# Kernel tuning notes

Hardware: AMD Instinct MI355X
Metric: run time of the kernel (lower is better)

The kernel has to match this reference:

```python
import jax, jax.numpy as jnp
import numpy as np

B, S, D_IN = 4, 2048, 1024
D_OUT, H = 1024, 16
HD = D_OUT // H  # head_dim = 64

def setup_inputs() -> dict:
    key = jax.random.key(0)
    ks = jax.random.split(key, 6)
    scale_in = 1.0 / np.sqrt(D_IN)
    scale_out = 1.0 / np.sqrt(D_OUT)
    return {
        "x": jax.random.normal(ks[0], (B, S, D_IN), dtype=jnp.float32),
        "Wq": jax.random.uniform(ks[1], (D_OUT, D_IN), jnp.float32, -scale_in, scale_in),
        "Wk": jax.random.uniform(ks[2], (D_OUT, D_IN), jnp.float32, -scale_in, scale_in),
        "Wv": jax.random.uniform(ks[3], (D_OUT, D_IN), jnp.float32, -scale_in, scale_in),
        "Wo": jax.random.uniform(ks[4], (D_OUT, D_OUT), jnp.float32, -scale_out, scale_out),
        "bo": jax.random.uniform(ks[5], (D_OUT,), jnp.float32, -scale_out, scale_out),
    }

def reference(x, Wq, Wk, Wv, Wo, bo):
    b, s, _ = x.shape
    # projections (nn.Linear: x @ W.T), split into heads -> [b, h, s, hd]
    def proj(W):
        return jnp.einsum('bsd,ed->bse', x, W).reshape(b, s, H, HD).transpose(0, 2, 1, 3)
    q, k, v = proj(Wq), proj(Wk), proj(Wv)
    # full score matrix [b, h, s, s] with causal mask, scaled softmax
    scores = jnp.einsum('bhqd,bhkd->bhqk', q, k)
    causal = jnp.tril(jnp.ones((s, s), dtype=bool))
    scores = jnp.where(causal, scores, -jnp.inf)
    attn = jax.nn.softmax(scores / np.sqrt(HD), axis=-1)
    # dropout p=0.0 -> identity
    ctx = jnp.einsum('bhqk,bhkd->bqhd', attn, v).reshape(b, s, D_OUT)
    return jnp.einsum('bsd,ed->bse', ctx, Wo) + bo
```

## Files before the change

kernel.cpp:

```cpp
#include <hip/hip_runtime.h>
#include <cstdint>
#include <cstddef>

#define S_LEN   2048
#define D_MODEL 1024
#define N_HEADS 16
#define HEAD_DIM 64
#define BATCH   4
#define M_ROWS  (BATCH * S_LEN)

typedef _Float16 half8  __attribute__((ext_vector_type(8)));
typedef _Float16 half4v __attribute__((ext_vector_type(4)));
typedef float    float4v __attribute__((ext_vector_type(4)));

#define AS1 __attribute__((address_space(1)))
#define AS3 __attribute__((address_space(3)))

#define QSCL 0.1803368801111832f

__device__ __forceinline__ int swz(int row, int byteInRow) {
    return row * 128 + ((((byteInRow >> 4) ^ (row & 7)) << 4)) + (byteInRow & 15);
}

__device__ __forceinline__ int vperm(int a) {
    return (a & 0x20) | ((a & 0x0C) << 1) | ((a & 0x10) >> 2) | (a & 3);
}

__global__ __launch_bounds__(256) void cvt_all(const float* __restrict__ x,
                                               const float* __restrict__ wq,
                                               const float* __restrict__ wk,
                                               const float* __restrict__ wv,
                                               const float* __restrict__ wo,
                                               _Float16* __restrict__ dst) {
    const int NX = M_ROWS * D_MODEL / 4;
    const int NW = D_MODEL * D_MODEL / 4;
    int i = blockIdx.x * 256 + threadIdx.x;
    int j = i;
    const float4v* src;
    if (j < NX) src = (const float4v*)x;
    else {
        j -= NX;
        if (j < NW) src = (const float4v*)wq;
        else { j -= NW;
            if (j < NW) src = (const float4v*)wk;
            else { j -= NW;
                if (j < NW) src = (const float4v*)wv;
                else { j -= NW; src = (const float4v*)wo; }
            }
        }
    }
    float4v v = src[j];
    half4v h;
    h[0] = (_Float16)v[0]; h[1] = (_Float16)v[1];
    h[2] = (_Float16)v[2]; h[3] = (_Float16)v[3];
    ((half4v*)dst)[i] = h;
}

#define GK   1024
#define GNT  16
#define BUFB 49152
#define GEMM_LDS (3 * BUFB)

template <int MODE>
__global__ __launch_bounds__(512, 2) void gemm8p(const _Float16* __restrict__ A,
                                                 const _Float16* __restrict__ Bw,
                                                 _Float16* __restrict__ O1,
                                                 _Float16* __restrict__ O2,
                                                 float* __restrict__ Of,
                                                 const float* __restrict__ bias,
                                                 int N) {
    extern __shared__ char smem[];

    const int tid  = threadIdx.x;
    const int wave = tid >> 6;
    const int lane = tid & 63;
    const int quad = lane >> 4;
    const int l16  = lane & 15;
    const int wm   = wave >> 1;
    const int wn   = wave & 1;

    const int rowBase = blockIdx.x * 256;
    const int colBase = blockIdx.y * 128;

    const int srow = tid >> 3;
    const int csw  = ((tid & 7) ^ (srow & 7)) * 8;
    const _Float16* aS[4];
    const _Float16* bS[2];
#pragma unroll
    for (int i = 0; i < 4; ++i)
        aS[i] = A + (size_t)(rowBase + i * 64 + srow) * GK + csw;
#pragma unroll
    for (int j = 0; j < 2; ++j)
        bS[j] = Bw + (size_t)(colBase + j * 64 + srow) * GK + csw;
    const int dstOff = tid * 16;

    auto stage = [&](int kt, int part) {
        char* base = smem + (kt % 3) * BUFB;
        const size_t ko = (size_t)kt * 64;
        if (part == 0) {
            __builtin_amdgcn_global_load_lds((const AS1 void*)(aS[0] + ko),
                (AS3 void*)(base + 0 * 8192 + dstOff), 16, 0, 0);
            __builtin_amdgcn_global_load_lds((const AS1 void*)(aS[1] + ko),
                (AS3 void*)(base + 1 * 8192 + dstOff), 16, 0, 0);
            __builtin_amdgcn_global_load_lds((const AS1 void*)(bS[0] + ko),
                (AS3 void*)(base + 32768 + dstOff), 16, 0, 0);
        } else {
            __builtin_amdgcn_global_load_lds((const AS1 void*)(aS[2] + ko),
                (AS3 void*)(base + 2 * 8192 + dstOff), 16, 0, 0);
            __builtin_amdgcn_global_load_lds((const AS1 void*)(aS[3] + ko),
                (AS3 void*)(base + 3 * 8192 + dstOff), 16, 0, 0);
            __builtin_amdgcn_global_load_lds((const AS1 void*)(bS[1] + ko),
                (AS3 void*)(base + 32768 + 8192 + dstOff), 16, 0, 0);
        }
    };

    const int aRow = (wm * 64 + l16) * 128;
    const int bRow = (wn * 64 + l16) * 128;
    int swzk[2];
    swzk[0] = ((quad)     ^ (l16 & 7)) << 4;
    swzk[1] = ((quad + 4) ^ (l16 & 7)) << 4;

    float4v acc[4][4] = {};

    stage(0, 0); stage(0, 1); stage(1, 0); stage(1, 1);
    asm volatile("s_waitcnt vmcnt(6)" ::: "memory");
    __builtin_amdgcn_s_barrier();

#pragma unroll
    for (int kt = 0; kt < GNT; ++kt) {
        const char* Ab = smem + (kt % 3) * BUFB;
        const char* Bb = Ab + 32768;
#pragma unroll
        for (int ks = 0; ks < 2; ++ks) {
            half8 af[4], bf[4];
#pragma unroll
            for (int mi = 0; mi < 4; ++mi)
                af[mi] = *(const half8*)(Ab + aRow + mi * 2048 + swzk[ks]);
#pragma unroll
            for (int ni = 0; ni < 4; ++ni)
                bf[ni] = *(const half8*)(Bb + bRow + ni * 2048 + swzk[ks]);
            if (kt + 2 < GNT) stage(kt + 2, ks);
            __builtin_amdgcn_s_barrier();
            asm volatile("s_waitcnt lgkmcnt(0)" ::: "memory");
            __builtin_amdgcn_sched_barrier(0);
            __builtin_amdgcn_s_setprio(1);
#pragma unroll
            for (int mi = 0; mi < 4; ++mi)
#pragma unroll
                for (int ni = 0; ni < 4; ++ni)
                    acc[mi][ni] = __builtin_amdgcn_mfma_f32_16x16x32_f16(
                        af[mi], bf[ni], acc[mi][ni], 0, 0, 0);
            __builtin_amdgcn_s_setprio(0);
            if (ks == 1) {
                if (kt + 2 < GNT) {
                    asm volatile("s_waitcnt vmcnt(6)" ::: "memory");
                } else if (kt + 1 < GNT) {
                    asm volatile("s_waitcnt vmcnt(0)" ::: "memory");
                }
            }
            __builtin_amdgcn_s_barrier();
        }
    }

    const int rowOff = wm * 64;
    const int colOff = wn * 64;
#pragma unroll
    for (int mi = 0; mi < 4; ++mi)
#pragma unroll
        for (int ni = 0; ni < 4; ++ni) {
            const int col = colBase + colOff + ni * 16 + l16;
#pragma unroll
            for (int i = 0; i < 4; ++i) {
                const int row = rowBase + rowOff + mi * 16 + quad * 4 + i;
                float v = acc[mi][ni][i];
                if (MODE == 0) {
                    int b_ = row >> 11, s_ = row & 2047;
                    int proj = col >> 10, d = col & 1023;
                    int h_ = d >> 6, hd = d & 63;
                    _Float16* dst = proj ? O2 : O1;
                    if (proj == 0) v *= QSCL;
                    dst[(((size_t)(b_ * 16 + h_) * 2048 + s_) << 6) + hd] = (_Float16)v;
                } else if (MODE == 1) {
                    int h_ = row >> 6, hd = row & 63;
                    int b_ = col >> 11, s_ = col & 2047;
                    int sp = (s_ & ~63) | vperm(s_ & 63);
                    O1[(((size_t)(b_ * 16 + h_) * 64 + hd) << 11) + sp] = (_Float16)v;
                } else {
                    Of[(size_t)row * N + col] = v + bias[col];
                }
            }
        }
}

template <bool MASKED>
__device__ __forceinline__ void softmax_side(const float4v (&sT)[2][4], int krow0,
                                             int qt, int quad, int c,
                                             half8 (&pf)[2][2], float4v (&ol)[2],
                                             half8 ones) {
#pragma unroll
    for (int s = 0; s < 2; ++s) {
        const int qrow = qt + s * 16 + c;
#pragma unroll
        for (int kk = 0; kk < 2; ++kk) {
            float e[2][4];
#pragma unroll
            for (int jh = 0; jh < 2; ++jh) {
                const int nt = 2 * kk + jh;
#pragma unroll
                for (int i = 0; i < 4; ++i) {
                    float ev = __builtin_amdgcn_exp2f(sT[s][nt][i]);
                    if (MASKED)
                        ev = (krow0 + nt * 16 + quad * 4 + i <= qrow) ? ev : 0.0f;
                    e[jh][i] = ev;
                }
            }
            auto p0 = __builtin_amdgcn_cvt_pkrtz(e[0][0], e[0][1]);
            auto p1 = __builtin_amdgcn_cvt_pkrtz(e[0][2], e[0][3]);
            auto p2 = __builtin_amdgcn_cvt_pkrtz(e[1][0], e[1][1]);
            auto p3 = __builtin_amdgcn_cvt_pkrtz(e[1][2], e[1][3]);
            half8 pfv;
            pfv[0] = p0[0]; pfv[1] = p0[1]; pfv[2] = p1[0]; pfv[3] = p1[1];
            pfv[4] = p2[0]; pfv[5] = p2[1]; pfv[6] = p3[0]; pfv[7] = p3[1];
            pf[s][kk] = pfv;
            ol[s] = __builtin_amdgcn_mfma_f32_16x16x32_f16(pfv, ones, ol[s], 0, 0, 0);
        }
    }
}

__global__ __launch_bounds__(256, 2) void attn_flash8(const _Float16* __restrict__ Q,
                                                      const _Float16* __restrict__ Kg,
                                                      const _Float16* __restrict__ Vt,
                                                      _Float16* __restrict__ Ctx) {
    __shared__ __align__(16) _Float16 Ks[2 * 64 * 64];
    __shared__ __align__(16) _Float16 Vs[2 * 64 * 64];

    const int tid  = threadIdx.x;
    const int wave = tid >> 6;
    const int lane = tid & 63;
    const int quad = lane >> 4;
    const int c    = lane & 15;

    const int h    = blockIdx.x & 15;
    const int bb   = blockIdx.x >> 4;
    const int pair = blockIdx.y;

    const int qA  = pair * 128 + wave * 32;
    const int qB  = (15 - pair) * 128 + wave * 32;
    const int nkb = (16 - pair) * 2;

    const _Float16* Qb  = Q  + ((size_t)(bb * 16 + h) << 17);
    const _Float16* Kb  = Kg + ((size_t)(bb * 16 + h) << 17);
    const _Float16* Vtb = Vt + ((size_t)(bb * 16 + h) << 17);

    half8 qfA[2][2], qfB[2][2];
#pragma unroll
    for (int s = 0; s < 2; ++s) {
        const _Float16* qa = Qb + (size_t)(qA + s * 16 + c) * 64;
        qfA[s][0] = *(const half8*)(qa + quad * 8);
        qfA[s][1] = *(const half8*)(qa + 32 + quad * 8);
        const _Float16* qb = Qb + (size_t)(qB + s * 16 + c) * 64;
        qfB[s][0] = *(const half8*)(qb + quad * 8);
        qfB[s][1] = *(const half8*)(qb + 32 + quad * 8);
    }

    size_t koff[2], voff[2];
#pragma unroll
    for (int it = 0; it < 2; ++it) {
        int F = it * 4096 + tid * 16;
        int r = F >> 7;
        int blk = (tid & 7) ^ (r & 7);
        koff[it] = (size_t)r * 64 + blk * 8;
        voff[it] = (size_t)r * 2048 + blk * 8;
    }

    float4v oB[2][4] = {}, oA[2][4] = {};
    float4v olB[2] = {}, olA[2] = {};
    half8 ones;
#pragma unroll
    for (int i = 0; i < 8; ++i) ones[i] = (_Float16)1.0f;

    auto stage = [&](int kb, int buf) {
        const size_t kbase = (size_t)kb * 64 * 64;
#pragma unroll
        for (int it = 0; it < 2; ++it) {
            __builtin_amdgcn_global_load_lds(
                (const AS1 void*)(Kb + kbase + koff[it]),
                (AS3 void*)((char*)Ks + buf * 8192 + it * 4096 + wave * 1024), 16, 0, 0);
            __builtin_amdgcn_global_load_lds(
                (const AS1 void*)(Vtb + kb * 64 + voff[it]),
                (AS3 void*)((char*)Vs + buf * 8192 + it * 4096 + wave * 1024), 16, 0, 0);
        }
    };

    const int g0 = ((quad ^ (c & 7)) << 4);
    const int g1 = (((quad ^ 4) ^ (c & 7)) << 4);

    stage(0, 0);
    for (int kb = 0; kb < nkb; ++kb) {
        __syncthreads();
        if (kb + 1 < nkb) stage(kb + 1, (kb + 1) & 1);

        const char* base  = (const char*)Ks + (kb & 1) * 8192;
        const char* vbase = (const char*)Vs + (kb & 1) * 8192;
        const char* b0 = base + c * 128 + g0;
        const char* b1 = base + c * 128 + g1;
        const int krow0 = kb * 64;
        const bool aB = krow0 <= qB + 31;
        const bool aA = krow0 <= qA + 31;

        half8 kfr[4][2];
#pragma unroll
        for (int nt = 0; nt < 4; ++nt) {
            kfr[nt][0] = *(const half8*)(b0 + nt * 2048);
            kfr[nt][1] = *(const half8*)(b1 + nt * 2048);
        }

        half8 pfB[2][2], pfA[2][2];
        if (aB) {
            float4v sT[2][4] = {};
            __builtin_amdgcn_s_setprio(1);
#pragma unroll
            for (int nt = 0; nt < 4; ++nt)
#pragma unroll
                for (int s = 0; s < 2; ++s) {
                    sT[s][nt] = __builtin_amdgcn_mfma_f32_16x16x32_f16(
                        kfr[nt][0], qfB[s][0], sT[s][nt], 0, 0, 0);
                    sT[s][nt] = __builtin_amdgcn_mfma_f32_16x16x32_f16(
                        kfr[nt][1], qfB[s][1], sT[s][nt], 0, 0, 0);
                }
            __builtin_amdgcn_s_setprio(0);
            if (krow0 + 63 <= qB)
                softmax_side<false>(sT, krow0, qB, quad, c, pfB, olB, ones);
            else
                softmax_side<true >(sT, krow0, qB, quad, c, pfB, olB, ones);
        }
        if (aA) {
            float4v sT[2][4] = {};
            __builtin_amdgcn_s_setprio(1);
#pragma unroll
            for (int nt = 0; nt < 4; ++nt)
#pragma unroll
                for (int s = 0; s < 2; ++s) {
                    sT[s][nt] = __builtin_amdgcn_mfma_f32_16x16x32_f16(
                        kfr[nt][0], qfA[s][0], sT[s][nt], 0, 0, 0);
                    sT[s][nt] = __builtin_amdgcn_mfma_f32_16x16x32_f16(
                        kfr[nt][1], qfA[s][1], sT[s][nt], 0, 0, 0);
                }
            __builtin_amdgcn_s_setprio(0);
            if (krow0 + 63 <= qA)
                softmax_side<false>(sT, krow0, qA, quad, c, pfA, olA, ones);
            else
                softmax_side<true >(sT, krow0, qA, quad, c, pfA, olA, ones);
        }

        const char* v0 = vbase + c * 128 + g0;
        const char* v1 = vbase + c * 128 + g1;
#pragma unroll
        for (int kk = 0; kk < 2; ++kk) {
            const char* vb = kk ? v1 : v0;
#pragma unroll
            for (int dt = 0; dt < 4; ++dt) {
                half8 vf = *(const half8*)(vb + dt * 2048);
                if (aB) {
                    oB[0][dt] = __builtin_amdgcn_mfma_f32_16x16x32_f16(
                        pfB[0][kk], vf, oB[0][dt], 0, 0, 0);
                    oB[1][dt] = __builtin_amdgcn_mfma_f32_16x16x32_f16(
                        pfB[1][kk], vf, oB[1][dt], 0, 0, 0);
                }
                if (aA) {
                    oA[0][dt] = __builtin_amdgcn_mfma_f32_16x16x32_f16(
                        pfA[0][kk], vf, oA[0][dt], 0, 0, 0);
                    oA[1][dt] = __builtin_amdgcn_mfma_f32_16x16x32_f16(
                        pfA[1][kk], vf, oA[1][dt], 0, 0, 0);
                }
            }
        }
    }

#pragma unroll
    for (int t = 0; t < 2; ++t) {
        const int qt = t ? qB : qA;
#pragma unroll
        for (int s = 0; s < 2; ++s) {
#pragma unroll
            for (int i = 0; i < 4; ++i) {
                const float lsum = t ? olB[s][i] : olA[s][i];
                const float inv = 1.0f / lsum;
                const int row_g = qt + s * 16 + quad * 4 + i;
                _Float16* dst = Ctx + (size_t)(bb * 2048 + row_g) * 1024 + h * 64;
#pragma unroll
                for (int dt = 0; dt < 4; ++dt) {
                    const float ov = t ? oB[s][dt][i] : oA[s][dt][i];
                    dst[dt * 16 + c] = (_Float16)(ov * inv);
                }
            }
        }
    }
}

extern "C" void kernel_launch(void* const* d_in, const int* in_sizes, int n_in,
                              void* d_out, int out_size, void* d_ws, size_t ws_size,
                              hipStream_t stream) {
    const float* x  = (const float*)d_in[0];
    const float* Wq = (const float*)d_in[1];
    const float* Wk = (const float*)d_in[2];
    const float* Wv = (const float*)d_in[3];
    const float* Wo = (const float*)d_in[4];
    const float* bo = (const float*)d_in[5];
    float* out = (float*)d_out;

    _Float16* Xh   = (_Float16*)d_ws;
    _Float16* Wqkh = Xh + (size_t)M_ROWS * D_MODEL;
    _Float16* Wvh  = Wqkh + (size_t)2 * D_MODEL * D_MODEL;
    _Float16* Woh  = Wvh + (size_t)D_MODEL * D_MODEL;
    _Float16* Qh   = Woh + (size_t)D_MODEL * D_MODEL;
    _Float16* Kh   = Qh + (size_t)M_ROWS * D_MODEL;
    _Float16* Vth  = Kh + (size_t)M_ROWS * D_MODEL;
    _Float16* Ch   = Vth + (size_t)M_ROWS * D_MODEL;

    static bool s_init = false;
    if (!s_init) {
        hipFuncSetAttribute((const void*)gemm8p<0>,
                            hipFuncAttributeMaxDynamicSharedMemorySize, GEMM_LDS);
        hipFuncSetAttribute((const void*)gemm8p<1>,
                            hipFuncAttributeMaxDynamicSharedMemorySize, GEMM_LDS);
        hipFuncSetAttribute((const void*)gemm8p<2>,
                            hipFuncAttributeMaxDynamicSharedMemorySize, GEMM_LDS);
        s_init = true;
    }

    const int TOT4 = (M_ROWS * D_MODEL + 4 * D_MODEL * D_MODEL) / 4;
    cvt_all<<<TOT4 / 256, 256, 0, stream>>>(x, Wq, Wk, Wv, Wo, Xh);

    gemm8p<0><<<dim3(M_ROWS / 256, 2048 / 128), 512, GEMM_LDS, stream>>>(
        Xh, Wqkh, Qh, Kh, nullptr, nullptr, 2048);
    gemm8p<1><<<dim3(D_MODEL / 256, M_ROWS / 128), 512, GEMM_LDS, stream>>>(
        Wvh, Xh, Vth, nullptr, nullptr, nullptr, M_ROWS);

    attn_flash8<<<dim3(64, 8), 256, 0, stream>>>(Qh, Kh, Vth, Ch);

    gemm8p<2><<<dim3(M_ROWS / 256, D_MODEL / 128), 512, GEMM_LDS, stream>>>(
        Ch, Woh, nullptr, nullptr, out, bo, D_MODEL);
}
```

Measured before the change: 157.0 us.

## Halve per-wave query rows in flash attention to double blocks and occupancy

```diff
diff --git a/kernel.cpp b/kernel.cpp
--- a/kernel.cpp
+++ b/kernel.cpp
@@ -193,41 +193,38 @@
 }
 
 template <bool MASKED>
-__device__ __forceinline__ void softmax_side(const float4v (&sT)[2][4], int krow0,
-                                             int qt, int quad, int c,
-                                             half8 (&pf)[2][2], float4v (&ol)[2],
-                                             half8 ones) {
-#pragma unroll
-    for (int s = 0; s < 2; ++s) {
-        const int qrow = qt + s * 16 + c;
-#pragma unroll
-        for (int kk = 0; kk < 2; ++kk) {
-            float e[2][4];
-#pragma unroll
-            for (int jh = 0; jh < 2; ++jh) {
-                const int nt = 2 * kk + jh;
-#pragma unroll
-                for (int i = 0; i < 4; ++i) {
-                    float ev = __builtin_amdgcn_exp2f(sT[s][nt][i]);
-                    if (MASKED)
-                        ev = (krow0 + nt * 16 + quad * 4 + i <= qrow) ? ev : 0.0f;
-                    e[jh][i] = ev;
-                }
-            }
-            auto p0 = __builtin_amdgcn_cvt_pkrtz(e[0][0], e[0][1]);
-            auto p1 = __builtin_amdgcn_cvt_pkrtz(e[0][2], e[0][3]);
-            auto p2 = __builtin_amdgcn_cvt_pkrtz(e[1][0], e[1][1]);
-            auto p3 = __builtin_amdgcn_cvt_pkrtz(e[1][2], e[1][3]);
-            half8 pfv;
-            pfv[0] = p0[0]; pfv[1] = p0[1]; pfv[2] = p1[0]; pfv[3] = p1[1];
-            pfv[4] = p2[0]; pfv[5] = p2[1]; pfv[6] = p3[0]; pfv[7] = p3[1];
-            pf[s][kk] = pfv;
-            ol[s] = __builtin_amdgcn_mfma_f32_16x16x32_f16(pfv, ones, ol[s], 0, 0, 0);
-        }
-    }
-}
-
-__global__ __launch_bounds__(256, 2) void attn_flash8(const _Float16* __restrict__ Q,
+__device__ __forceinline__ void softmax_one(const float4v (&sT)[4], int krow0,
+                                            int qt, int quad, int c,
+                                            half8 (&pf)[2], float4v& ol,
+                                            half8 ones) {
+    const int qrow = qt + c;
+#pragma unroll
+    for (int kk = 0; kk < 2; ++kk) {
+        float e[2][4];
+#pragma unroll
+        for (int jh = 0; jh < 2; ++jh) {
+            const int nt = 2 * kk + jh;
+#pragma unroll
+            for (int i = 0; i < 4; ++i) {
+                float ev = __builtin_amdgcn_exp2f(sT[nt][i]);
+                if (MASKED)
+                    ev = (krow0 + nt * 16 + quad * 4 + i <= qrow) ? ev : 0.0f;
+                e[jh][i] = ev;
+            }
+        }
+        auto p0 = __builtin_amdgcn_cvt_pkrtz(e[0][0], e[0][1]);
+        auto p1 = __builtin_amdgcn_cvt_pkrtz(e[0][2], e[0][3]);
+        auto p2 = __builtin_amdgcn_cvt_pkrtz(e[1][0], e[1][1]);
+        auto p3 = __builtin_amdgcn_cvt_pkrtz(e[1][2], e[1][3]);
+        half8 pfv;
+        pfv[0] = p0[0]; pfv[1] = p0[1]; pfv[2] = p1[0]; pfv[3] = p1[1];
+        pfv[4] = p2[0]; pfv[5] = p2[1]; pfv[6] = p3[0]; pfv[7] = p3[1];
+        pf[kk] = pfv;
+        ol = __builtin_amdgcn_mfma_f32_16x16x32_f16(pfv, ones, ol, 0, 0, 0);
+    }
+}
+
+__global__ __launch_bounds__(256, 4) void attn_flash9(const _Float16* __restrict__ Q,
                                                       const _Float16* __restrict__ Kg,
                                                       const _Float16* __restrict__ Vt,
                                                       _Float16* __restrict__ Ctx) {
@@ -242,25 +239,27 @@
 
     const int h    = blockIdx.x & 15;
     const int bb   = blockIdx.x >> 4;
-    const int pair = blockIdx.y;
-
-    const int qA  = pair * 128 + wave * 32;
-    const int qB  = (15 - pair) * 128 + wave * 32;
-    const int nkb = (16 - pair) * 2;
+    const int y    = blockIdx.y;
+    const int hp   = (y < 8) ? y : 23 - y;
+    const int pair = hp >> 1;
+    const int hf   = hp & 1;
+
+    const int qA  = pair * 128 + hf * 64 + wave * 16;
+    const int qB  = (15 - pair) * 128 + hf * 64 + wave * 16;
+    const int nkb = (15 - pair) * 2 + hf + 1;
 
     const _Float16* Qb  = Q  + ((size_t)(bb * 16 + h) << 17);
     const _Float16* Kb  = Kg + ((size_t)(bb * 16 + h) << 17);
     const _Float16* Vtb = Vt + ((size_t)(bb * 16 + h) << 17);
 
-    half8 qfA[2][2], qfB[2][2];
-#pragma unroll
-    for (int s = 0; s < 2; ++s) {
-        const _Float16* qa = Qb + (size_t)(qA + s * 16 + c) * 64;
-        qfA[s][0] = *(const half8*)(qa + quad * 8);
-        qfA[s][1] = *(const half8*)(qa + 32 + quad * 8);
-        const _Float16* qb = Qb + (size_t)(qB + s * 16 + c) * 64;
-        qfB[s][0] = *(const half8*)(qb + quad * 8);
-        qfB[s][1] = *(const half8*)(qb + 32 + quad * 8);
+    half8 qfA[2], qfB[2];
+    {
+        const _Float16* qa = Qb + (size_t)(qA + c) * 64;
+        qfA[0] = *(const half8*)(qa + quad * 8);
+        qfA[1] = *(const half8*)(qa + 32 + quad * 8);
+        const _Float16* qb = Qb + (size_t)(qB + c) * 64;
+        qfB[0] = *(const half8*)(qb + quad * 8);
+        qfB[1] = *(const half8*)(qb + 32 + quad * 8);
     }
 
     size_t koff[2], voff[2];
@@ -273,8 +272,8 @@
         voff[it] = (size_t)r * 2048 + blk * 8;
     }
 
-    float4v oB[2][4] = {}, oA[2][4] = {};
-    float4v olB[2] = {}, olA[2] = {};
+    float4v oB[4] = {}, oA[4] = {};
+    float4v olB = {}, olA = {};
     half8 ones;
 #pragma unroll
     for (int i = 0; i < 8; ++i) ones[i] = (_Float16)1.0f;
@@ -305,8 +304,8 @@
         const char* b0 = base + c * 128 + g0;
         const char* b1 = base + c * 128 + g1;
         const int krow0 = kb * 64;
-        const bool aB = krow0 <= qB + 31;
-        const bool aA = krow0 <= qA + 31;
+        const bool aB = krow0 <= qB + 15;
+        const bool aA = krow0 <= qA + 15;
 
         half8 kfr[4][2];
 #pragma unroll
@@ -315,84 +314,73 @@
             kfr[nt][1] = *(const half8*)(b1 + nt * 2048);
         }
 
-        half8 pfB[2][2], pfA[2][2];
+        half8 pfB[2], pfA[2];
         if (aB) {
-            float4v sT[2][4] = {};
+            float4v sT[4] = {};
             __builtin_amdgcn_s_setprio(1);
 #pragma unroll
-            for (int nt = 0; nt < 4; ++nt)
-#pragma unroll
-                for (int s = 0; s < 2; ++s) {
-                    sT[s][nt] = __builtin_amdgcn_mfma_f32_16x16x32_f16(
-                        kfr[nt][0], qfB[s][0], sT[s][nt], 0, 0, 0);
-                    sT[s][nt] = __builtin_amdgcn_mfma_f32_16x16x32_f16(
-                        kfr[nt][1], qfB[s][1], sT[s][nt], 0, 0, 0);
-                }
+            for (int nt = 0; nt < 4; ++nt) {
+                sT[nt] = __builtin_amdgcn_mfma_f32_16x16x32_f16(
+                    kfr[nt][0], qfB[0], sT[nt], 0, 0, 0);
+                sT[nt] = __builtin_amdgcn_mfma_f32_16x16x32_f16(
+                    kfr[nt][1], qfB[1], sT[nt], 0, 0, 0);
+            }
             __builtin_amdgcn_s_setprio(0);
             if (krow0 + 63 <= qB)
-                softmax_side<false>(sT, krow0, qB, quad, c, pfB, olB, ones);
+                softmax_one<false>(sT, krow0, qB, quad, c, pfB, olB, ones);
             else
-                softmax_side<true >(sT, krow0, qB, quad, c, pfB, olB, ones);
+                softmax_one<true >(sT, krow0, qB, quad, c, pfB, olB, ones);
         }
         if (aA) {
-            float4v sT[2][4] = {};
+            float4v sT[4] = {};
             __builtin_amdgcn_s_setprio(1);
 #pragma unroll
-            for (int nt = 0; nt < 4; ++nt)
-#pragma unroll
-                for (int s = 0; s < 2; ++s) {
-                    sT[s][nt] = __builtin_amdgcn_mfma_f32_16x16x32_f16(
-                        kfr[nt][0], qfA[s][0], sT[s][nt], 0, 0, 0);
-                    sT[s][nt] = __builtin_amdgcn_mfma_f32_16x16x32_f16(
-                        kfr[nt][1], qfA[s][1], sT[s][nt], 0, 0, 0);
-                }
+            for (int nt = 0; nt < 4; ++nt) {
+                sT[nt] = __builtin_amdgcn_mfma_f32_16x16x32_f16(
+                    kfr[nt][0], qfA[0], sT[nt], 0, 0, 0);
+                sT[nt] = __builtin_amdgcn_mfma_f32_16x16x32_f16(
+                    kfr[nt][1], qfA[1], sT[nt], 0, 0, 0);
+            }
             __builtin_amdgcn_s_setprio(0);
             if (krow0 + 63 <= qA)
-                softmax_side<false>(sT, krow0, qA, quad, c, pfA, olA, ones);
+                softmax_one<false>(sT, krow0, qA, quad, c, pfA, olA, ones);
             else
-                softmax_side<true >(sT, krow0, qA, quad, c, pfA, olA, ones);
+                softmax_one<true >(sT, krow0, qA, quad, c, pfA, olA, ones);
         }
 
         const char* v0 = vbase + c * 128 + g0;
         const char* v1 = vbase + c * 128 + g1;
+        __builtin_amdgcn_s_setprio(1);
 #pragma unroll
         for (int kk = 0; kk < 2; ++kk) {
             const char* vb = kk ? v1 : v0;
 #pragma unroll
             for (int dt = 0; dt < 4; ++dt) {
                 half8 vf = *(const half8*)(vb + dt * 2048);
-                if (aB) {
-                    oB[0][dt] = __builtin_amdgcn_mfma_f32_16x16x32_f16(
-                        pfB[0][kk], vf, oB[0][dt], 0, 0, 0);
-                    oB[1][dt] = __builtin_amdgcn_mfma_f32_16x16x32_f16(
-                        pfB[1][kk], vf, oB[1][dt], 0, 0, 0);
-                }
-                if (aA) {
-                    oA[0][dt] = __builtin_amdgcn_mfma_f32_16x16x32_f16(
-                        pfA[0][kk], vf, oA[0][dt], 0, 0, 0);
-                    oA[1][dt] = __builtin_amdgcn_mfma_f32_16x16x32_f16(
-                        pfA[1][kk], vf, oA[1][dt], 0, 0, 0);
-                }
-            }
-        }
+                if (aB)
+                    oB[dt] = __builtin_amdgcn_mfma_f32_16x16x32_f16(
+                        pfB[kk], vf, oB[dt], 0, 0, 0);
+                if (aA)
+                    oA[dt] = __builtin_amdgcn_mfma_f32_16x16x32_f16(
+                        pfA[kk], vf, oA[dt], 0, 0, 0);
+            }
+        }
+        __builtin_amdgcn_s_setprio(0);
     }
 
 #pragma unroll
     for (int t = 0; t < 2; ++t) {
         const int qt = t ? qB : qA;
 #pragma unroll
-        for (int s = 0; s < 2; ++s) {
-#pragma unroll
-            for (int i = 0; i < 4; ++i) {
-                const float lsum = t ? olB[s][i] : olA[s][i];
-                const float inv = 1.0f / lsum;
-                const int row_g = qt + s * 16 + quad * 4 + i;
-                _Float16* dst = Ctx + (size_t)(bb * 2048 + row_g) * 1024 + h * 64;
-#pragma unroll
-                for (int dt = 0; dt < 4; ++dt) {
-                    const float ov = t ? oB[s][dt][i] : oA[s][dt][i];
-                    dst[dt * 16 + c] = (_Float16)(ov * inv);
-                }
+        for (int i = 0; i < 4; ++i) {
+            const float lsum = t ? olB[i] : olA[i];
+            const float inv = 1.0f / lsum;
+            const int row_g = qt + quad * 4 + i;
+            _Float16* dst = Ctx + (size_t)(bb * 2048 + row_g) * 1024 + h * 64;
+#pragma unroll
+            for (int dt = 0; dt < 4; ++dt) {
+                const float ov = t ? oB[dt][i] : oA[dt][i];
+                dst[dt * 16 + c] = (_Float16)(ov * inv);
             }
         }
     }
@@ -437,7 +425,7 @@
     gemm8p<1><<<dim3(D_MODEL / 256, M_ROWS / 128), 512, GEMM_LDS, stream>>>(
         Wvh, Xh, Vth, nullptr, nullptr, nullptr, M_ROWS);
 
-    attn_flash8<<<dim3(64, 8), 256, 0, stream>>>(Qh, Kh, Vth, Ch);
+    attn_flash9<<<dim3(64, 16), 256, 0, stream>>>(Qh, Kh, Vth, Ch);
 
     gemm8p<2><<<dim3(M_ROWS / 256, D_MODEL / 128), 512, GEMM_LDS, stream>>>(
         Ch, Woh, nullptr, nullptr, out, bo, D_MODEL);
```

Result: slower. 179.5 us (+14.3%).
